# Kernel tuning notes

Measured on AMD Instinct MI355X. Metric: run time of the kernel, lower is better.

Reference implementation:

```python
import jax, jax.numpy as jnp
import numpy as np

BATCH = 65536
DIM = 512
NUM_CLASSES = 1000
NUM_OLD = 500  # old_classes == set(range(NUM_OLD))


def setup_inputs() -> dict:
    key = jax.random.key(0)
    k1, k2, k3 = jax.random.split(key, 3)
    embeddings = jax.random.normal(k1, (BATCH, DIM), dtype=jnp.float32)
    centroids = jax.random.normal(k2, (NUM_CLASSES, DIM), dtype=jnp.float32)
    labels = jax.random.randint(k3, (BATCH,), 0, NUM_CLASSES, dtype=jnp.int64 if jax.config.jax_enable_x64 else jnp.int32)
    return {"embeddings": embeddings, "centroids": centroids, "labels": labels, "num_old": NUM_OLD}


def reference(embeddings, centroids, labels, num_old):
    # Fused gather + per-sample MSE + masked mean (replaces the per-sample Python loop).
    gathered = centroids[labels]                                  # [B, D]
    per_sample = jnp.mean((embeddings - gathered) ** 2, axis=-1)  # [B], F.mse_loss per sample
    # Original accumulates dis.detach(): the loss value carries no gradient.
    per_sample = jax.lax.stop_gradient(per_sample)
    mask = labels < num_old                                       # label in old_classes
    count = jnp.sum(mask)
    total = jnp.sum(jnp.where(mask, per_sample, jnp.float32(0.0)))
    # if count == 0: return raw (zero) loss, else mean
    loss = jnp.where(count == 0, total, total / jnp.maximum(count, 1).astype(total.dtype))
    return loss
```

## Files before the change

kernel.cpp:

```cpp
#include <hip/hip_runtime.h>

constexpr int kDim = 512;
constexpr int kF4PerRow = kDim / 4;

__device__ __forceinline__ float sqdiff8(float4 e0, float4 e1, float4 c0, float4 c1) {
    float d, t;
    d = e0.x - c0.x; t  = d * d;
    d = e0.y - c0.y; t += d * d;
    d = e0.z - c0.z; t += d * d;
    d = e0.w - c0.w; t += d * d;
    d = e1.x - c1.x; t += d * d;
    d = e1.y - c1.y; t += d * d;
    d = e1.z - c1.z; t += d * d;
    d = e1.w - c1.w; t += d * d;
    return t;
}

__global__ __launch_bounds__(256) void mse_masked_kernel(
    const float* __restrict__ emb,
    const float* __restrict__ cen,
    const int* __restrict__ labels,
    const int* __restrict__ num_old_p,
    int batch,
    float* __restrict__ ws_sum,
    unsigned int* __restrict__ ws_cnt)
{
    const int num_old = *num_old_p;
    const int lane = threadIdx.x & 63;
    const int wid  = threadIdx.x >> 6;
    const int wpb  = blockDim.x >> 6;
    const int gwave = blockIdx.x * wpb + wid;
    const int nwave = gridDim.x * wpb;

    const float4* __restrict__ emb4 = (const float4*)emb;
    const float4* __restrict__ cen4 = (const float4*)cen;

    float acc = 0.0f;
    unsigned int cnt = 0;

    for (int chunk = gwave * 64; chunk < batch; chunk += nwave * 64) {
        const int idx = chunk + lane;
        const int mylab = (idx < batch) ? labels[idx] : 0x7fffffff;
        unsigned long long m = __ballot(mylab < num_old);
        cnt += (unsigned int)__popcll(m);

        while (__popcll(m) >= 4) {
            const int b0 = __builtin_ctzll(m); m &= m - 1;
            const int b1 = __builtin_ctzll(m); m &= m - 1;
            const int b2 = __builtin_ctzll(m); m &= m - 1;
            const int b3 = __builtin_ctzll(m); m &= m - 1;
            const int l0 = __shfl(mylab, b0, 64);
            const int l1 = __shfl(mylab, b1, 64);
            const int l2 = __shfl(mylab, b2, 64);
            const int l3 = __shfl(mylab, b3, 64);

            const float4* e0p = emb4 + (size_t)(chunk + b0) * kF4PerRow;
            const float4* e1p = emb4 + (size_t)(chunk + b1) * kF4PerRow;
            const float4* e2p = emb4 + (size_t)(chunk + b2) * kF4PerRow;
            const float4* e3p = emb4 + (size_t)(chunk + b3) * kF4PerRow;
            const float4* c0p = cen4 + (size_t)l0 * kF4PerRow;
            const float4* c1p = cen4 + (size_t)l1 * kF4PerRow;
            const float4* c2p = cen4 + (size_t)l2 * kF4PerRow;
            const float4* c3p = cen4 + (size_t)l3 * kF4PerRow;

            float4 ea0 = e0p[lane], eb0 = e0p[lane + 64];
            float4 ea1 = e1p[lane], eb1 = e1p[lane + 64];
            float4 ea2 = e2p[lane], eb2 = e2p[lane + 64];
            float4 ea3 = e3p[lane], eb3 = e3p[lane + 64];
            float4 ca0 = c0p[lane], cb0 = c0p[lane + 64];
            float4 ca1 = c1p[lane], cb1 = c1p[lane + 64];
            float4 ca2 = c2p[lane], cb2 = c2p[lane + 64];
            float4 ca3 = c3p[lane], cb3 = c3p[lane + 64];

            acc += sqdiff8(ea0, eb0, ca0, cb0);
            acc += sqdiff8(ea1, eb1, ca1, cb1);
            acc += sqdiff8(ea2, eb2, ca2, cb2);
            acc += sqdiff8(ea3, eb3, ca3, cb3);
        }
        while (m) {
            const int b = __builtin_ctzll(m); m &= m - 1;
            const int l = __shfl(mylab, b, 64);
            const float4* ep = emb4 + (size_t)(chunk + b) * kF4PerRow;
            const float4* cp = cen4 + (size_t)l * kF4PerRow;
            float4 e0 = ep[lane], e1 = ep[lane + 64];
            float4 c0 = cp[lane], c1 = cp[lane + 64];
            acc += sqdiff8(e0, e1, c0, c1);
        }
    }

    #pragma unroll
    for (int off = 32; off > 0; off >>= 1)
        acc += __shfl_xor(acc, off, 64);

    __shared__ float        s_sum[4];
    __shared__ unsigned int s_cnt[4];
    if (lane == 0) { s_sum[wid] = acc; s_cnt[wid] = cnt; }
    __syncthreads();

    if (threadIdx.x == 0) {
        float        bs = 0.0f;
        unsigned int bc = 0u;
        for (int i = 0; i < wpb; ++i) { bs += s_sum[i]; bc += s_cnt[i]; }
        ws_sum[blockIdx.x] = bs;
        ws_cnt[blockIdx.x] = bc;
    }
}

__global__ __launch_bounds__(256) void finalize_kernel(
    const float* __restrict__ ws_sum,
    const unsigned int* __restrict__ ws_cnt,
    int nparts,
    float* __restrict__ out)
{
    const int t = threadIdx.x;
    float        s = (t < nparts) ? ws_sum[t] : 0.0f;
    unsigned int c = (t < nparts) ? ws_cnt[t] : 0u;

    #pragma unroll
    for (int off = 32; off > 0; off >>= 1) {
        s += __shfl_xor(s, off, 64);
        c += __shfl_xor(c, off, 64);
    }
    __shared__ float        ls[4];
    __shared__ unsigned int lc[4];
    const int lane = t & 63, wid = t >> 6;
    if (lane == 0) { ls[wid] = s; lc[wid] = c; }
    __syncthreads();
    if (t == 0) {
        float        ts = ls[0] + ls[1] + ls[2] + ls[3];
        unsigned int tc = lc[0] + lc[1] + lc[2] + lc[3];
        const float total = ts * (1.0f / (float)kDim);
        out[0] = (tc == 0u) ? total : total / (float)tc;
    }
}

extern "C" void kernel_launch(void* const* d_in, const int* in_sizes, int n_in,
                              void* d_out, int out_size, void* d_ws, size_t ws_size,
                              hipStream_t stream) {
    const float* emb       = (const float*)d_in[0];
    const float* cen       = (const float*)d_in[1];
    const int*   labels    = (const int*)d_in[2];
    const int*   num_old_p = (const int*)d_in[3];

    const int batch = in_sizes[2];

    const int blocks = 256;
    float*        ws_sum = (float*)d_ws;
    unsigned int* ws_cnt = (unsigned int*)((char*)d_ws + blocks * sizeof(float));

    mse_masked_kernel<<<blocks, 256, 0, stream>>>(emb, cen, labels, num_old_p,
                                                  batch, ws_sum, ws_cnt);
    finalize_kernel<<<1, 256, 0, stream>>>(ws_sum, ws_cnt, blocks, (float*)d_out);
}
```

Before: 187.3 us.

## Split each 64-row chunk across a block's waves and raise grid size

Each block now processes one 64-row chunk per iteration. Its four waves interleave over the masked rows, with wave w taking every fourth set bit starting at offset w, instead of each wave owning whole chunks. The grid grows from 256 blocks to up to 2048, and the finalize kernel loops to handle more partials. Embedding loads become nontemporal so the reused centroid rows are not evicted from cache, and the kernel adds an occupancy hint. The aim is to spread the memory-bound gather across more CUs and keep more loads in flight. In exchange, every wave now redundantly reads labels and computes the ballot for each chunk.

```diff
diff --git a/kernel.cpp b/kernel.cpp
--- a/kernel.cpp
+++ b/kernel.cpp
@@ -3,20 +3,16 @@
 constexpr int kDim = 512;
 constexpr int kF4PerRow = kDim / 4;
 
-__device__ __forceinline__ float sqdiff8(float4 e0, float4 e1, float4 c0, float4 c1) {
-    float d, t;
-    d = e0.x - c0.x; t  = d * d;
-    d = e0.y - c0.y; t += d * d;
-    d = e0.z - c0.z; t += d * d;
-    d = e0.w - c0.w; t += d * d;
-    d = e1.x - c1.x; t += d * d;
-    d = e1.y - c1.y; t += d * d;
-    d = e1.z - c1.z; t += d * d;
-    d = e1.w - c1.w; t += d * d;
-    return t;
+typedef float f32x4 __attribute__((ext_vector_type(4)));
+
+__device__ __forceinline__ float sqd8(f32x4 e0, f32x4 e1, f32x4 c0, f32x4 c1) {
+    f32x4 d0 = e0 - c0;
+    f32x4 d1 = e1 - c1;
+    f32x4 s  = d0 * d0 + d1 * d1;
+    return s.x + s.y + s.z + s.w;
 }
 
-__global__ __launch_bounds__(256) void mse_masked_kernel(
+__global__ __launch_bounds__(256, 4) void mse_masked_kernel(
     const float* __restrict__ emb,
     const float* __restrict__ cen,
     const int* __restrict__ labels,
@@ -28,63 +24,76 @@
     const int num_old = *num_old_p;
     const int lane = threadIdx.x & 63;
     const int wid  = threadIdx.x >> 6;
-    const int wpb  = blockDim.x >> 6;
-    const int gwave = blockIdx.x * wpb + wid;
-    const int nwave = gridDim.x * wpb;
 
-    const float4* __restrict__ emb4 = (const float4*)emb;
-    const float4* __restrict__ cen4 = (const float4*)cen;
+    const f32x4* __restrict__ emb4 = (const f32x4*)emb;
+    const f32x4* __restrict__ cen4 = (const f32x4*)cen;
 
     float acc = 0.0f;
     unsigned int cnt = 0;
 
-    for (int chunk = gwave * 64; chunk < batch; chunk += nwave * 64) {
+    for (int c = blockIdx.x; c * 64 < batch; c += gridDim.x) {
+        const int chunk = c * 64;
         const int idx = chunk + lane;
         const int mylab = (idx < batch) ? labels[idx] : 0x7fffffff;
         unsigned long long m = __ballot(mylab < num_old);
-        cnt += (unsigned int)__popcll(m);
+        if (wid == 0) cnt += (unsigned int)__popcll(m);
 
-        while (__popcll(m) >= 4) {
-            const int b0 = __builtin_ctzll(m); m &= m - 1;
-            const int b1 = __builtin_ctzll(m); m &= m - 1;
-            const int b2 = __builtin_ctzll(m); m &= m - 1;
-            const int b3 = __builtin_ctzll(m); m &= m - 1;
+        for (int s = 0; s < wid; ++s) m &= m - 1;
+
+        while (__popcll(m) >= 13) {
+            unsigned long long t = m;
+            const int b0 = __builtin_ctzll(t);
+            t &= t - 1; t &= t - 1; t &= t - 1; t &= t - 1;
+            const int b1 = __builtin_ctzll(t);
+            t &= t - 1; t &= t - 1; t &= t - 1; t &= t - 1;
+            const int b2 = __builtin_ctzll(t);
+            t &= t - 1; t &= t - 1; t &= t - 1; t &= t - 1;
+            const int b3 = __builtin_ctzll(t);
+            t &= t - 1; t &= t - 1; t &= t - 1; t &= t - 1;
+            m = t;
+
             const int l0 = __shfl(mylab, b0, 64);
             const int l1 = __shfl(mylab, b1, 64);
             const int l2 = __shfl(mylab, b2, 64);
             const int l3 = __shfl(mylab, b3, 64);
 
-            const float4* e0p = emb4 + (size_t)(chunk + b0) * kF4PerRow;
-            const float4* e1p = emb4 + (size_t)(chunk + b1) * kF4PerRow;
-            const float4* e2p = emb4 + (size_t)(chunk + b2) * kF4PerRow;
-            const float4* e3p = emb4 + (size_t)(chunk + b3) * kF4PerRow;
-            const float4* c0p = cen4 + (size_t)l0 * kF4PerRow;
-            const float4* c1p = cen4 + (size_t)l1 * kF4PerRow;
-            const float4* c2p = cen4 + (size_t)l2 * kF4PerRow;
-            const float4* c3p = cen4 + (size_t)l3 * kF4PerRow;
+            const f32x4* e0p = emb4 + (size_t)(chunk + b0) * kF4PerRow;
+            const f32x4* e1p = emb4 + (size_t)(chunk + b1) * kF4PerRow;
+            const f32x4* e2p = emb4 + (size_t)(chunk + b2) * kF4PerRow;
+            const f32x4* e3p = emb4 + (size_t)(chunk + b3) * kF4PerRow;
+            const f32x4* c0p = cen4 + (size_t)l0 * kF4PerRow;
+            const f32x4* c1p = cen4 + (size_t)l1 * kF4PerRow;
+            const f32x4* c2p = cen4 + (size_t)l2 * kF4PerRow;
+            const f32x4* c3p = cen4 + (size_t)l3 * kF4PerRow;
 
-            float4 ea0 = e0p[lane], eb0 = e0p[lane + 64];
-            float4 ea1 = e1p[lane], eb1 = e1p[lane + 64];
-            float4 ea2 = e2p[lane], eb2 = e2p[lane + 64];
-            float4 ea3 = e3p[lane], eb3 = e3p[lane + 64];
-            float4 ca0 = c0p[lane], cb0 = c0p[lane + 64];
-            float4 ca1 = c1p[lane], cb1 = c1p[lane + 64];
-            float4 ca2 = c2p[lane], cb2 = c2p[lane + 64];
-            float4 ca3 = c3p[lane], cb3 = c3p[lane + 64];
+            f32x4 ea0 = __builtin_nontemporal_load(e0p + lane);
+            f32x4 eb0 = __builtin_nontemporal_load(e0p + lane + 64);
+            f32x4 ea1 = __builtin_nontemporal_load(e1p + lane);
+            f32x4 eb1 = __builtin_nontemporal_load(e1p + lane + 64);
+            f32x4 ea2 = __builtin_nontemporal_load(e2p + lane);
+            f32x4 eb2 = __builtin_nontemporal_load(e2p + lane + 64);
+            f32x4 ea3 = __builtin_nontemporal_load(e3p + lane);
+            f32x4 eb3 = __builtin_nontemporal_load(e3p + lane + 64);
+            f32x4 ca0 = c0p[lane], cb0 = c0p[lane + 64];
+            f32x4 ca1 = c1p[lane], cb1 = c1p[lane + 64];
+            f32x4 ca2 = c2p[lane], cb2 = c2p[lane + 64];
+            f32x4 ca3 = c3p[lane], cb3 = c3p[lane + 64];
 
-            acc += sqdiff8(ea0, eb0, ca0, cb0);
-            acc += sqdiff8(ea1, eb1, ca1, cb1);
-            acc += sqdiff8(ea2, eb2, ca2, cb2);
-            acc += sqdiff8(ea3, eb3, ca3, cb3);
+            acc += sqd8(ea0, eb0, ca0, cb0);
+            acc += sqd8(ea1, eb1, ca1, cb1);
+            acc += sqd8(ea2, eb2, ca2, cb2);
+            acc += sqd8(ea3, eb3, ca3, cb3);
         }
         while (m) {
-            const int b = __builtin_ctzll(m); m &= m - 1;
+            const int b = __builtin_ctzll(m);
+            m &= m - 1; m &= m - 1; m &= m - 1; m &= m - 1;
             const int l = __shfl(mylab, b, 64);
-            const float4* ep = emb4 + (size_t)(chunk + b) * kF4PerRow;
-            const float4* cp = cen4 + (size_t)l * kF4PerRow;
-            float4 e0 = ep[lane], e1 = ep[lane + 64];
-            float4 c0 = cp[lane], c1 = cp[lane + 64];
-            acc += sqdiff8(e0, e1, c0, c1);
+            const f32x4* ep = emb4 + (size_t)(chunk + b) * kF4PerRow;
+            const f32x4* cp = cen4 + (size_t)l * kF4PerRow;
+            f32x4 e0 = __builtin_nontemporal_load(ep + lane);
+            f32x4 e1 = __builtin_nontemporal_load(ep + lane + 64);
+            f32x4 c0 = cp[lane], c1 = cp[lane + 64];
+            acc += sqd8(e0, e1, c0, c1);
         }
     }
 
@@ -100,6 +109,7 @@
     if (threadIdx.x == 0) {
         float        bs = 0.0f;
         unsigned int bc = 0u;
+        const int wpb = blockDim.x >> 6;
         for (int i = 0; i < wpb; ++i) { bs += s_sum[i]; bc += s_cnt[i]; }
         ws_sum[blockIdx.x] = bs;
         ws_cnt[blockIdx.x] = bc;
@@ -113,8 +123,9 @@
     float* __restrict__ out)
 {
     const int t = threadIdx.x;
-    float        s = (t < nparts) ? ws_sum[t] : 0.0f;
-    unsigned int c = (t < nparts) ? ws_cnt[t] : 0u;
+    float        s = 0.0f;
+    unsigned int c = 0u;
+    for (int i = t; i < nparts; i += 256) { s += ws_sum[i]; c += ws_cnt[i]; }
 
     #pragma unroll
     for (int off = 32; off > 0; off >>= 1) {
@@ -144,7 +155,8 @@
 
     const int batch = in_sizes[2];
 
-    const int blocks = 256;
+    int blocks = (batch + 63) / 64;
+    if (blocks > 2048) blocks = 2048;
     float*        ws_sum = (float*)d_ws;
     unsigned int* ws_cnt = (unsigned int*)((char*)d_ws + blocks * sizeof(float));
 
```

After: 178.0 us. -4.9%, faster.
